# Kernel optimization log

Hardware: AMD Instinct MI355X
Metric: run time of the kernel (lower is better)

The kernel has to match this reference:

```python
import jax, jax.numpy as jnp
import numpy as np

H = 128        # num_hidden
NIN = 384      # num_in
FF = 4 * H
SCALE = 30.0
EPS = 1e-5


def _gelu(x):
    return jax.nn.gelu(x, approximate=False)


def _layernorm(x, g, b):
    mu = jnp.mean(x, axis=-1, keepdims=True)
    var = jnp.var(x, axis=-1, keepdims=True)
    return (x - mu) * jax.lax.rsqrt(var + EPS) * g + b


def setup_inputs() -> dict:
    key = jax.random.key(0)
    ks = jax.random.split(key, 12)
    B, N, K = 4, 2048, 48
    s = lambda fan_in: 1.0 / np.sqrt(fan_in)
    inp = {
        "h_V": jax.random.normal(ks[0], (B, N, H), jnp.float32),
        "h_E": jax.random.normal(ks[1], (B, N, K, NIN), jnp.float32),
        "mask_V": jnp.ones((B, N), jnp.float32),
        "mask_attend": jnp.ones((B, N, K), jnp.float32),
        "W1_w": jax.random.uniform(ks[2], (H + NIN, H), jnp.float32, -s(H + NIN), s(H + NIN)),
        "W1_b": jnp.zeros((H,), jnp.float32),
        "W2_w": jax.random.uniform(ks[3], (H, H), jnp.float32, -s(H), s(H)),
        "W2_b": jnp.zeros((H,), jnp.float32),
        "W3_w": jax.random.uniform(ks[4], (H, H), jnp.float32, -s(H), s(H)),
        "W3_b": jnp.zeros((H,), jnp.float32),
        "Win_w": jax.random.uniform(ks[5], (H, FF), jnp.float32, -s(H), s(H)),
        "Win_b": jnp.zeros((FF,), jnp.float32),
        "Wout_w": jax.random.uniform(ks[6], (FF, H), jnp.float32, -s(FF), s(FF)),
        "Wout_b": jnp.zeros((H,), jnp.float32),
        "ln1_g": jnp.ones((H,), jnp.float32),
        "ln1_b": jnp.zeros((H,), jnp.float32),
        "ln2_g": jnp.ones((H,), jnp.float32),
        "ln2_b": jnp.zeros((H,), jnp.float32),
    }
    return inp


def reference(h_V, h_E, mask_V, mask_attend,
              W1_w, W1_b, W2_w, W2_b, W3_w, W3_b,
              Win_w, Win_b, Wout_w, Wout_b,
              ln1_g, ln1_b, ln2_g, ln2_b):
    B, N, K, _ = h_E.shape
    # expand node feats over K neighbors and concat with edge feats -> [B,N,K,H+NIN]
    h_V_expand = jnp.broadcast_to(h_V[:, :, None, :], (B, N, K, h_V.shape[-1]))
    h_EV = jnp.concatenate([h_V_expand, h_E], axis=-1)
    # edge MLP: 3 linears, 2 GELUs
    h_message = _gelu(h_EV @ W1_w + W1_b)
    h_message = _gelu(h_message @ W2_w + W2_b)
    h_message = h_message @ W3_w + W3_b
    h_message = mask_attend[..., None] * h_message
    dh = jnp.sum(h_message, axis=-2) / SCALE  # [B,N,H]
    h = _layernorm(h_V + dh, ln1_g, ln1_b)
    # position-wise FFN
    dh = _gelu(h @ Win_w + Win_b) @ Wout_w + Wout_b
    h = _layernorm(h + dh, ln2_g, ln2_b)
    h = mask_V[..., None] * h
    return h
```

## Files before the change

### kernel.cpp

```cpp
#include <hip/hip_runtime.h>
#include <hip/hip_bf16.h>

#define Hh    128
#define NINc  384
#define KN    48
#define FFd   512
#define NNODE 8192

typedef __attribute__((ext_vector_type(8))) short short8v;
typedef __attribute__((ext_vector_type(4))) float f32x4;

__device__ __forceinline__ short f2bf1(float f){
  union { __hip_bfloat16 h; short s; } c; c.h = __float2bfloat16(f);
  return c.s;
}
__device__ __forceinline__ unsigned pk_bf16(float lo, float hi){
  union { __hip_bfloat162 h; unsigned u; } c;
  c.h = __float22bfloat162_rn(make_float2(lo, hi));
  return c.u;
}

__device__ __forceinline__ float gelu_f(float x){
  float t = 0.7978845608028654f * x * (1.0f + 0.044715f * x * x);
  float e = __expf(2.0f * t);
  return x * (1.0f - 1.0f / (e + 1.0f));
}

__device__ __forceinline__ void bar_lds(){
  asm volatile("s_waitcnt lgkmcnt(0)\n\ts_barrier" ::: "memory");
}

__global__ void prep_weights(const float* __restrict__ W1, const float* __restrict__ W2,
                             const float* __restrict__ W3, const float* __restrict__ Win,
                             const float* __restrict__ Wout,
                             short* __restrict__ w1vT, short* __restrict__ w1p,
                             short* __restrict__ w2p,  short* __restrict__ w3p,
                             short* __restrict__ winT, short* __restrict__ woutT)
{
  int i = blockIdx.x * 256 + threadIdx.x;
  if (i < 16384){ int n = i / 128, k = i % 128; w1vT[i] = f2bf1(W1[k*128 + n]); return; }
  i -= 16384;
  if (i < 49152){
    int n = i / 6144, r = i % 6144;
    int ks = r / 512, r2 = r % 512;
    int lane = r2 / 8, j = r2 % 8;
    int qq = lane >> 4, arow = lane & 15;
    w1p[i] = f2bf1(W1[(128 + ks*32 + qq*8 + j)*128 + n*16 + arow]); return;
  }
  i -= 49152;
  if (i < 16384){
    int n = i / 2048, r = i % 2048;
    int ks = r / 512, r2 = r % 512;
    int lane = r2 / 8, j = r2 % 8;
    int qq = lane >> 4, arow = lane & 15;
    w2p[i] = f2bf1(W2[(ks*32 + qq*8 + j)*128 + n*16 + arow]); return;
  }
  i -= 16384;
  if (i < 16384){
    int n = i / 2048, r = i % 2048;
    int ks = r / 512, r2 = r % 512;
    int lane = r2 / 8, j = r2 % 8;
    int qq = lane >> 4, arow = lane & 15;
    w3p[i] = f2bf1(W3[(ks*32 + qq*8 + j)*128 + n*16 + arow]); return;
  }
  i -= 16384;
  if (i < 65536){ int n = i / 128, k = i % 128; winT[i] = f2bf1(Win[k*512 + n]); return; }
  i -= 65536;
  if (i < 65536){ int n = i / 512, k = i % 512; woutT[i] = f2bf1(Wout[k*128 + n]); return; }
}

__global__ __launch_bounds__(256,4) void np_kernel(
    const float* __restrict__ hV, const short* __restrict__ w1vT,
    const float* __restrict__ b1, float* __restrict__ npart)
{
  const int row0 = blockIdx.x * 32;
  const int tid = threadIdx.x, lane = tid & 63, wv = tid >> 6;
  __shared__ __attribute__((aligned(16))) short Xs[32][Hh + 8];

  const float4* src = (const float4*)(hV + (size_t)row0 * Hh);
  #pragma unroll
  for (int j = 0; j < 4; ++j){
    int idx = tid + 256*j;
    int r = idx >> 5, c4 = idx & 31;
    float4 v = src[idx];
    *(uint2*)&Xs[r][c4*4] = make_uint2(pk_bf16(v.x,v.y), pk_bf16(v.z,v.w));
  }
  __syncthreads();

  const int arow = lane & 15, kgrp = (lane >> 4) * 8;
  const int col0 = wv * 32, ccol = lane & 15, crow0 = (lane >> 4) * 4;

  f32x4 acc[2][2];
  #pragma unroll
  for (int m = 0; m < 2; ++m) for (int n = 0; n < 2; ++n) acc[m][n] = (f32x4){0.f,0.f,0.f,0.f};

  const short8v* Bw = (const short8v*)w1vT;
  #pragma unroll
  for (int ks = 0; ks < 4; ++ks){
    int kb = ks*32 + kgrp;
    short8v b0 = Bw[(col0 + arow)*16      + (kb >> 3)];
    short8v b1f = Bw[(col0 + 16 + arow)*16 + (kb >> 3)];
    #pragma unroll
    for (int m = 0; m < 2; ++m){
      short8v a = *(const short8v*)&Xs[m*16 + arow][kb];
      acc[m][0] = __builtin_amdgcn_mfma_f32_16x16x32_bf16(a, b0,  acc[m][0], 0,0,0);
      acc[m][1] = __builtin_amdgcn_mfma_f32_16x16x32_bf16(a, b1f, acc[m][1], 0,0,0);
    }
  }
  #pragma unroll
  for (int m = 0; m < 2; ++m) for (int n = 0; n < 2; ++n){
    int colg = col0 + n*16 + ccol;
    float bb = b1[colg];
    #pragma unroll
    for (int r = 0; r < 4; ++r)
      npart[(size_t)(row0 + m*16 + crow0 + r)*Hh + colg] = acc[m][n][r] + bb;
  }
}

__global__ __launch_bounds__(256,4) void edge_kernel(
    const float* __restrict__ hE, const float* __restrict__ hV,
    const float* __restrict__ maskA, const float* __restrict__ npart,
    const short* __restrict__ w1p, const short* __restrict__ w2p,
    const short* __restrict__ w3p,
    const float* __restrict__ b2, const float* __restrict__ b3,
    float* __restrict__ out)
{
  const int node = blockIdx.x;
  const int tid = threadIdx.x, lane = tid & 63, wv = tid >> 6;
  const int e = lane & 15, q = lane >> 4;
  const int n0 = wv * 32;

  __shared__ __attribute__((aligned(16))) short Et[KN][NINc + 8];
  short (*M1)[136] = (short (*)[136])&Et[0][0];
  short (*M2)[136] = (short (*)[136])(&Et[0][0] + KN*136);

  {
    const float4* src = (const float4*)(hE + (size_t)node * (KN*NINc));
    float4 pfa[9], pfb[9];
    #pragma unroll
    for (int j = 0; j < 9; ++j){
      pfa[j] = src[2*tid     + 512*j];
      pfb[j] = src[2*tid + 1 + 512*j];
    }
    #pragma unroll
    for (int j = 0; j < 9; ++j){
      int idx = 2*tid + 512*j;
      int r = idx / 96, c = idx - r*96;
      uint4 u;
      u.x = pk_bf16(pfa[j].x, pfa[j].y);
      u.y = pk_bf16(pfa[j].z, pfa[j].w);
      u.z = pk_bf16(pfb[j].x, pfb[j].y);
      u.w = pk_bf16(pfb[j].z, pfb[j].w);
      *(uint4*)&Et[r][c*4] = u;
    }
  }

  const float4 npv0 = *(const float4*)(npart + (size_t)node*Hh + n0 + 4*q);
  const float4 npv1 = *(const float4*)(npart + (size_t)node*Hh + n0 + 16 + 4*q);
  const float mk0 = maskA[node*KN + e];
  const float mk1 = maskA[node*KN + 16 + e];
  const float mk2 = maskA[node*KN + 32 + e];

  bar_lds();

  const f32x4 Z = (f32x4){0.f,0.f,0.f,0.f};

  #define WR_M(DST, ACC, ET, COLB, BV)  { short4 s;                 \
    s.x = f2bf1(gelu_f(ACC[0] + BV.x));                             \
    s.y = f2bf1(gelu_f(ACC[1] + BV.y));                             \
    s.z = f2bf1(gelu_f(ACC[2] + BV.z));                             \
    s.w = f2bf1(gelu_f(ACC[3] + BV.w));                             \
    *(short4*)&DST[16*ET + e][COLB + 4*q] = s; }

  f32x4 a00=Z, a10=Z, a20=Z, a01=Z, a11=Z, a21=Z;
  {
    const short8v* B1 = (const short8v*)w1p;
    #pragma unroll
    for (int ks = 0; ks < 12; ++ks){
      short8v f0 = B1[((2*wv  )*12 + ks)*64 + lane];
      short8v f1 = B1[((2*wv+1)*12 + ks)*64 + lane];
      int kb = ks*32 + q*8;
      short8v t0 = *(const short8v*)&Et[e][kb];
      short8v t1 = *(const short8v*)&Et[16 + e][kb];
      short8v t2 = *(const short8v*)&Et[32 + e][kb];
      a00 = __builtin_amdgcn_mfma_f32_16x16x32_bf16(f0, t0, a00, 0,0,0);
      a10 = __builtin_amdgcn_mfma_f32_16x16x32_bf16(f0, t1, a10, 0,0,0);
      a20 = __builtin_amdgcn_mfma_f32_16x16x32_bf16(f0, t2, a20, 0,0,0);
      a01 = __builtin_amdgcn_mfma_f32_16x16x32_bf16(f1, t0, a01, 0,0,0);
      a11 = __builtin_amdgcn_mfma_f32_16x16x32_bf16(f1, t1, a11, 0,0,0);
      a21 = __builtin_amdgcn_mfma_f32_16x16x32_bf16(f1, t2, a21, 0,0,0);
    }
  }
  bar_lds();

  const float4 b2v0 = *(const float4*)(b2 + n0 + 4*q);
  const float4 b2v1 = *(const float4*)(b2 + n0 + 16 + 4*q);

  {
    WR_M(M1, a00, 0, n0,      npv0)  WR_M(M1, a10, 1, n0,      npv0)
    WR_M(M1, a20, 2, n0,      npv0)  WR_M(M1, a01, 0, n0 + 16, npv1)
    WR_M(M1, a11, 1, n0 + 16, npv1)  WR_M(M1, a21, 2, n0 + 16, npv1)
  }
  bar_lds();

  {
    f32x4 c00=Z, c10=Z, c20=Z, c01=Z, c11=Z, c21=Z;
    const short8v* B2f = (const short8v*)w2p;
    #pragma unroll
    for (int ks = 0; ks < 4; ++ks){
      short8v f0 = B2f[((2*wv  )*4 + ks)*64 + lane];
      short8v f1 = B2f[((2*wv+1)*4 + ks)*64 + lane];
      int kb = ks*32 + q*8;
      short8v t0 = *(const short8v*)&M1[e][kb];
      short8v t1 = *(const short8v*)&M1[16 + e][kb];
      short8v t2 = *(const short8v*)&M1[32 + e][kb];
      c00 = __builtin_amdgcn_mfma_f32_16x16x32_bf16(f0, t0, c00, 0,0,0);
      c10 = __builtin_amdgcn_mfma_f32_16x16x32_bf16(f0, t1, c10, 0,0,0);
      c20 = __builtin_amdgcn_mfma_f32_16x16x32_bf16(f0, t2, c20, 0,0,0);
      c01 = __builtin_amdgcn_mfma_f32_16x16x32_bf16(f1, t0, c01, 0,0,0);
      c11 = __builtin_amdgcn_mfma_f32_16x16x32_bf16(f1, t1, c11, 0,0,0);
      c21 = __builtin_amdgcn_mfma_f32_16x16x32_bf16(f1, t2, c21, 0,0,0);
    }
    WR_M(M2, c00, 0, n0,      b2v0)  WR_M(M2, c10, 1, n0,      b2v0)
    WR_M(M2, c20, 2, n0,      b2v0)  WR_M(M2, c01, 0, n0 + 16, b2v1)
    WR_M(M2, c11, 1, n0 + 16, b2v1)  WR_M(M2, c21, 2, n0 + 16, b2v1)
  }

  const float4 b3v0 = *(const float4*)(b3 + n0 + 4*q);
  const float4 b3v1 = *(const float4*)(b3 + n0 + 16 + 4*q);
  const float4 hvv0 = *(const float4*)(hV + (size_t)node*Hh + n0 + 4*q);
  const float4 hvv1 = *(const float4*)(hV + (size_t)node*Hh + n0 + 16 + 4*q);

  bar_lds();

  {
    f32x4 d00=Z, d10=Z, d20=Z, d01=Z, d11=Z, d21=Z;
    const short8v* B3f = (const short8v*)w3p;
    #pragma unroll
    for (int ks = 0; ks < 4; ++ks){
      short8v f0 = B3f[((2*wv  )*4 + ks)*64 + lane];
      short8v f1 = B3f[((2*wv+1)*4 + ks)*64 + lane];
      int kb = ks*32 + q*8;
      short8v t0 = *(const short8v*)&M2[e][kb];
      short8v t1 = *(const short8v*)&M2[16 + e][kb];
      short8v t2 = *(const short8v*)&M2[32 + e][kb];
      d00 = __builtin_amdgcn_mfma_f32_16x16x32_bf16(f0, t0, d00, 0,0,0);
      d10 = __builtin_amdgcn_mfma_f32_16x16x32_bf16(f0, t1, d10, 0,0,0);
      d20 = __builtin_amdgcn_mfma_f32_16x16x32_bf16(f0, t2, d20, 0,0,0);
      d01 = __builtin_amdgcn_mfma_f32_16x16x32_bf16(f1, t0, d01, 0,0,0);
      d11 = __builtin_amdgcn_mfma_f32_16x16x32_bf16(f1, t1, d11, 0,0,0);
      d21 = __builtin_amdgcn_mfma_f32_16x16x32_bf16(f1, t2, d21, 0,0,0);
    }
    f32x4 v0, v1;
    #pragma unroll
    for (int r = 0; r < 4; ++r){
      v0[r] = (d00[r] + b3v0[r])*mk0 + (d10[r] + b3v0[r])*mk1 + (d20[r] + b3v0[r])*mk2;
      v1[r] = (d01[r] + b3v1[r])*mk0 + (d11[r] + b3v1[r])*mk1 + (d21[r] + b3v1[r])*mk2;
    }
    #pragma unroll
    for (int s = 1; s <= 8; s <<= 1){
      #pragma unroll
      for (int r = 0; r < 4; ++r){
        v0[r] += __shfl_xor(v0[r], s);
        v1[r] += __shfl_xor(v1[r], s);
      }
    }
    if (e == 0){
      float4 o0, o1;
      o0.x = hvv0.x + v0[0]*(1.0f/30.0f); o0.y = hvv0.y + v0[1]*(1.0f/30.0f);
      o0.z = hvv0.z + v0[2]*(1.0f/30.0f); o0.w = hvv0.w + v0[3]*(1.0f/30.0f);
      o1.x = hvv1.x + v1[0]*(1.0f/30.0f); o1.y = hvv1.y + v1[1]*(1.0f/30.0f);
      o1.z = hvv1.z + v1[2]*(1.0f/30.0f); o1.w = hvv1.w + v1[3]*(1.0f/30.0f);
      *(float4*)(out + (size_t)node*Hh + n0 + 4*q)      = o0;
      *(float4*)(out + (size_t)node*Hh + n0 + 16 + 4*q) = o1;
    }
  }
  #undef WR_M
}

__global__ __launch_bounds__(256,2) void ffn_kernel(
    const float* __restrict__ ln1g, const float* __restrict__ ln1b,
    const short* __restrict__ winT, const float* __restrict__ bin,
    const short* __restrict__ woutT, const float* __restrict__ bout,
    const float* __restrict__ ln2g, const float* __restrict__ ln2b,
    const float* __restrict__ maskV, float* __restrict__ io)
{
  const int row0 = blockIdx.x * 32;
  const int tid = threadIdx.x, lane = tid & 63, wv = tid >> 6;
  __shared__ __attribute__((aligned(16))) short Xs[32][Hh + 8];
  __shared__ __attribute__((aligned(16))) float Rs[32][Hh + 4];
  __shared__ __attribute__((aligned(16))) short Hs[32][FFd + 8];

  const int arow = lane & 15, kgrp = (lane >> 4) * 8;
  const int ccol = lane & 15, crow0 = (lane >> 4) * 4;

  {
    int r = tid >> 3, cb = (tid & 7) * 16;
    const float4* xp = (const float4*)(io + (size_t)(row0 + r)*Hh + cb);
    float xv[16];
    #pragma unroll
    for (int j = 0; j < 4; ++j){
      float4 v = xp[j];
      xv[j*4+0]=v.x; xv[j*4+1]=v.y; xv[j*4+2]=v.z; xv[j*4+3]=v.w;
    }
    float sum = 0.f, sq = 0.f;
    #pragma unroll
    for (int j = 0; j < 16; ++j){ sum += xv[j]; sq += xv[j]*xv[j]; }
    #pragma unroll
    for (int d = 1; d < 8; d <<= 1){ sum += __shfl_xor(sum, d); sq += __shfl_xor(sq, d); }
    float mu = sum * (1.0f/128.0f);
    float var = sq * (1.0f/128.0f) - mu*mu;
    float rstd = rsqrtf(var + 1e-5f);
    #pragma unroll
    for (int j = 0; j < 16; ++j){
      int c = cb + j;
      float xn = (xv[j] - mu) * rstd * ln1g[c] + ln1b[c];
      Xs[r][c] = f2bf1(xn);
      Rs[r][c] = xn;
    }
  }
  __syncthreads();

  {
    f32x4 acc[2][8];
    #pragma unroll
    for (int m = 0; m < 2; ++m) for (int n = 0; n < 8; ++n) acc[m][n] = (f32x4){0.f,0.f,0.f,0.f};
    const short8v* Bw = (const short8v*)winT;
    #pragma unroll
    for (int ks = 0; ks < 4; ++ks){
      int kb = ks*32 + kgrp;
      short8v a0 = *(const short8v*)&Xs[arow][kb];
      short8v a1 = *(const short8v*)&Xs[16 + arow][kb];
      #pragma unroll
      for (int n = 0; n < 8; ++n){
        short8v b = Bw[(wv*128 + n*16 + arow)*16 + (kb >> 3)];
        acc[0][n] = __builtin_amdgcn_mfma_f32_16x16x32_bf16(a0,b,acc[0][n],0,0,0);
        acc[1][n] = __builtin_amdgcn_mfma_f32_16x16x32_bf16(a1,b,acc[1][n],0,0,0);
      }
    }
    #pragma unroll
    for (int m = 0; m < 2; ++m) for (int n = 0; n < 8; ++n){
      int colg = wv*128 + n*16 + ccol;
      float bb = bin[colg];
      #pragma unroll
      for (int r = 0; r < 4; ++r)
        Hs[m*16 + crow0 + r][colg] = f2bf1(gelu_f(acc[m][n][r] + bb));
    }
  }
  __syncthreads();

  {
    f32x4 acc[2][2];
    #pragma unroll
    for (int m = 0; m < 2; ++m) for (int n = 0; n < 2; ++n) acc[m][n] = (f32x4){0.f,0.f,0.f,0.f};
    const short8v* Bw = (const short8v*)woutT;
    #pragma unroll
    for (int ks = 0; ks < 16; ++ks){
      int kb = ks*32 + kgrp;
      short8v a0 = *(const short8v*)&Hs[arow][kb];
      short8v a1 = *(const short8v*)&Hs[16 + arow][kb];
      short8v b0 = Bw[(wv*32 + arow)*64      + (kb >> 3)];
      short8v b1f = Bw[(wv*32 + 16 + arow)*64 + (kb >> 3)];
      acc[0][0] = __builtin_amdgcn_mfma_f32_16x16x32_bf16(a0,b0, acc[0][0],0,0,0);
      acc[1][0] = __builtin_amdgcn_mfma_f32_16x16x32_bf16(a1,b0, acc[1][0],0,0,0);
      acc[0][1] = __builtin_amdgcn_mfma_f32_16x16x32_bf16(a0,b1f,acc[0][1],0,0,0);
      acc[1][1] = __builtin_amdgcn_mfma_f32_16x16x32_bf16(a1,b1f,acc[1][1],0,0,0);
    }
    #pragma unroll
    for (int m = 0; m < 2; ++m) for (int n = 0; n < 2; ++n){
      int colg = wv*32 + n*16 + ccol;
      float bb = bout[colg];
      #pragma unroll
      for (int r = 0; r < 4; ++r){
        int rr = m*16 + crow0 + r;
        Rs[rr][colg] = Rs[rr][colg] + acc[m][n][r] + bb;
      }
    }
  }
  __syncthreads();

  {
    int r = tid >> 3, cb = (tid & 7) * 16;
    float xv[16];
    #pragma unroll
    for (int j = 0; j < 16; ++j) xv[j] = Rs[r][cb + j];
    float sum = 0.f, sq = 0.f;
    #pragma unroll
    for (int j = 0; j < 16; ++j){ sum += xv[j]; sq += xv[j]*xv[j]; }
    #pragma unroll
    for (int d = 1; d < 8; d <<= 1){ sum += __shfl_xor(sum, d); sq += __shfl_xor(sq, d); }
    float mu = sum * (1.0f/128.0f);
    float var = sq * (1.0f/128.0f) - mu*mu;
    float rstd = rsqrtf(var + 1e-5f);
    float mv = maskV[row0 + r];
    float* op = io + (size_t)(row0 + r)*Hh + cb;
    #pragma unroll
    for (int j = 0; j < 4; ++j){
      float4 o;
      o.x = ((xv[j*4+0] - mu)*rstd*ln2g[cb+j*4+0] + ln2b[cb+j*4+0]) * mv;
      o.y = ((xv[j*4+1] - mu)*rstd*ln2g[cb+j*4+1] + ln2b[cb+j*4+1]) * mv;
      o.z = ((xv[j*4+2] - mu)*rstd*ln2g[cb+j*4+2] + ln2b[cb+j*4+2]) * mv;
      o.w = ((xv[j*4+3] - mu)*rstd*ln2g[cb+j*4+3] + ln2b[cb+j*4+3]) * mv;
      ((float4*)op)[j] = o;
    }
  }
}

extern "C" void kernel_launch(void* const* d_in, const int* in_sizes, int n_in,
                              void* d_out, int out_size, void* d_ws, size_t ws_size,
                              hipStream_t stream)
{
  const float* hV    = (const float*)d_in[0];
  const float* hE    = (const float*)d_in[1];
  const float* maskV = (const float*)d_in[2];
  const float* maskA = (const float*)d_in[3];
  const float* W1w   = (const float*)d_in[4];
  const float* W1b   = (const float*)d_in[5];
  const float* W2w   = (const float*)d_in[6];
  const float* W2b   = (const float*)d_in[7];
  const float* W3w   = (const float*)d_in[8];
  const float* W3b   = (const float*)d_in[9];
  const float* Winw  = (const float*)d_in[10];
  const float* Winb  = (const float*)d_in[11];
  const float* Woutw = (const float*)d_in[12];
  const float* Woutb = (const float*)d_in[13];
  const float* l1g   = (const float*)d_in[14];
  const float* l1b   = (const float*)d_in[15];
  const float* l2g   = (const float*)d_in[16];
  const float* l2b   = (const float*)d_in[17];

  char* ws = (char*)d_ws;
  size_t off = 0;
  float* npart = (float*)(ws + off); off += (size_t)NNODE * Hh * 4;
  short* w1vT  = (short*)(ws + off); off += 16384*2;
  short* w1p   = (short*)(ws + off); off += 49152*2;
  short* w2p   = (short*)(ws + off); off += 16384*2;
  short* w3p   = (short*)(ws + off); off += 16384*2;
  short* winT  = (short*)(ws + off); off += 65536*2;
  short* woutT = (short*)(ws + off); off += 65536*2;
  if (ws_size < off) return;

  prep_weights<<<896, 256, 0, stream>>>(W1w, W2w, W3w, Winw, Woutw,
                                        w1vT, w1p, w2p, w3p, winT, woutT);
  np_kernel<<<NNODE/32, 256, 0, stream>>>(hV, w1vT, W1b, npart);
  edge_kernel<<<NNODE, 256, 0, stream>>>(hE, hV, maskA, npart,
                                         w1p, w2p, w3p, W2b, W3b, (float*)d_out);
  ffn_kernel<<<NNODE/32, 256, 0, stream>>>(l1g, l1b, winT, Winb, woutT, Woutb,
                                           l2g, l2b, maskV, (float*)d_out);
}
```

Before: 204.7 us.

## Warp-specialize edge kernel with producer waves double-buffering hE over persistent nodes

Edge kernel now processes 32 nodes per block with 512 threads: four producer waves load and bf16-convert the next node's hE into a double-buffered LDS tile while four consumer waves run the three-layer MLP on the current node. W1 fragments are held in registers across all nodes instead of reloaded per node. This aims to overlap global memory streaming with MFMA work, at the cost of a smaller grid (256 blocks), extra barriers per node, and heavy register use from the cached W1 fragments.

```diff
diff --git a/kernel.cpp b/kernel.cpp
--- a/kernel.cpp
+++ b/kernel.cpp
@@ -6,6 +6,8 @@
 #define KN    48
 #define FFd   512
 #define NNODE 8192
+#define NPB   32
+#define EGRID (NNODE/NPB)
 
 typedef __attribute__((ext_vector_type(8))) short short8v;
 typedef __attribute__((ext_vector_type(4))) float f32x4;
@@ -117,7 +119,7 @@
   }
 }
 
-__global__ __launch_bounds__(256,4) void edge_kernel(
+__global__ __launch_bounds__(512,2) void edge_kernel(
     const float* __restrict__ hE, const float* __restrict__ hV,
     const float* __restrict__ maskA, const float* __restrict__ npart,
     const short* __restrict__ w1p, const short* __restrict__ w2p,
@@ -125,45 +127,64 @@
     const float* __restrict__ b2, const float* __restrict__ b3,
     float* __restrict__ out)
 {
-  const int node = blockIdx.x;
+  const int base = blockIdx.x * NPB;
   const int tid = threadIdx.x, lane = tid & 63, wv = tid >> 6;
+  const bool cons = (wv < 4), prod = !cons;
   const int e = lane & 15, q = lane >> 4;
-  const int n0 = wv * 32;
-
-  __shared__ __attribute__((aligned(16))) short Et[KN][NINc + 8];
-  short (*M1)[136] = (short (*)[136])&Et[0][0];
-  short (*M2)[136] = (short (*)[136])(&Et[0][0] + KN*136);
-
-  {
-    const float4* src = (const float4*)(hE + (size_t)node * (KN*NINc));
-    float4 pfa[9], pfb[9];
+  const int n0 = (wv & 3) * 32;
+  const int tid2 = tid & 255;
+
+  __shared__ __attribute__((aligned(16))) short Et[2][KN][NINc + 8];
+  __shared__ __attribute__((aligned(16))) short M1[KN][136];
+  __shared__ __attribute__((aligned(16))) short M2[KN][136];
+
+  float4 pfa[9], pfb[9];
+  auto LOADP = [&](int nn){
+    const float4* src = (const float4*)(hE + (size_t)nn * (KN*NINc));
     #pragma unroll
     for (int j = 0; j < 9; ++j){
-      pfa[j] = src[2*tid     + 512*j];
-      pfb[j] = src[2*tid + 1 + 512*j];
-    }
+      pfa[j] = src[2*tid2     + 512*j];
+      pfb[j] = src[2*tid2 + 1 + 512*j];
+    }
+  };
+  auto STOREP = [&](int buf){
     #pragma unroll
     for (int j = 0; j < 9; ++j){
-      int idx = 2*tid + 512*j;
+      int idx = 2*tid2 + 512*j;
       int r = idx / 96, c = idx - r*96;
       uint4 u;
       u.x = pk_bf16(pfa[j].x, pfa[j].y);
       u.y = pk_bf16(pfa[j].z, pfa[j].w);
       u.z = pk_bf16(pfb[j].x, pfb[j].y);
       u.w = pk_bf16(pfb[j].z, pfb[j].w);
-      *(uint4*)&Et[r][c*4] = u;
-    }
-  }
-
-  const float4 npv0 = *(const float4*)(npart + (size_t)node*Hh + n0 + 4*q);
-  const float4 npv1 = *(const float4*)(npart + (size_t)node*Hh + n0 + 16 + 4*q);
-  const float mk0 = maskA[node*KN + e];
-  const float mk1 = maskA[node*KN + 16 + e];
-  const float mk2 = maskA[node*KN + 32 + e];
-
+      *(uint4*)&Et[buf][r][c*4] = u;
+    }
+  };
+
+  short8v w1f0[12], w1f1[12];
+  float4 b2v0, b2v1, b3v0, b3v1;
+  if (cons){
+    const short8v* B1 = (const short8v*)w1p;
+    #pragma unroll
+    for (int ks = 0; ks < 12; ++ks){
+      w1f0[ks] = B1[((2*(wv&3)  )*12 + ks)*64 + lane];
+      w1f1[ks] = B1[((2*(wv&3)+1)*12 + ks)*64 + lane];
+    }
+    b2v0 = *(const float4*)(b2 + n0 + 4*q);
+    b2v1 = *(const float4*)(b2 + n0 + 16 + 4*q);
+    b3v0 = *(const float4*)(b3 + n0 + 4*q);
+    b3v1 = *(const float4*)(b3 + n0 + 16 + 4*q);
+  }
+
+  if (prod){
+    LOADP(base);
+    STOREP(0);
+    LOADP(base + 1);
+  }
   bar_lds();
 
   const f32x4 Z = (f32x4){0.f,0.f,0.f,0.f};
+  int cur = 0;
 
   #define WR_M(DST, ACC, ET, COLB, BV)  { short4 s;                 \
     s.x = f2bf1(gelu_f(ACC[0] + BV.x));                             \
@@ -172,108 +193,113 @@
     s.w = f2bf1(gelu_f(ACC[3] + BV.w));                             \
     *(short4*)&DST[16*ET + e][COLB + 4*q] = s; }
 
-  f32x4 a00=Z, a10=Z, a20=Z, a01=Z, a11=Z, a21=Z;
-  {
-    const short8v* B1 = (const short8v*)w1p;
-    #pragma unroll
-    for (int ks = 0; ks < 12; ++ks){
-      short8v f0 = B1[((2*wv  )*12 + ks)*64 + lane];
-      short8v f1 = B1[((2*wv+1)*12 + ks)*64 + lane];
-      int kb = ks*32 + q*8;
-      short8v t0 = *(const short8v*)&Et[e][kb];
-      short8v t1 = *(const short8v*)&Et[16 + e][kb];
-      short8v t2 = *(const short8v*)&Et[32 + e][kb];
-      a00 = __builtin_amdgcn_mfma_f32_16x16x32_bf16(f0, t0, a00, 0,0,0);
-      a10 = __builtin_amdgcn_mfma_f32_16x16x32_bf16(f0, t1, a10, 0,0,0);
-      a20 = __builtin_amdgcn_mfma_f32_16x16x32_bf16(f0, t2, a20, 0,0,0);
-      a01 = __builtin_amdgcn_mfma_f32_16x16x32_bf16(f1, t0, a01, 0,0,0);
-      a11 = __builtin_amdgcn_mfma_f32_16x16x32_bf16(f1, t1, a11, 0,0,0);
-      a21 = __builtin_amdgcn_mfma_f32_16x16x32_bf16(f1, t2, a21, 0,0,0);
-    }
-  }
-  bar_lds();
-
-  const float4 b2v0 = *(const float4*)(b2 + n0 + 4*q);
-  const float4 b2v1 = *(const float4*)(b2 + n0 + 16 + 4*q);
-
-  {
-    WR_M(M1, a00, 0, n0,      npv0)  WR_M(M1, a10, 1, n0,      npv0)
-    WR_M(M1, a20, 2, n0,      npv0)  WR_M(M1, a01, 0, n0 + 16, npv1)
-    WR_M(M1, a11, 1, n0 + 16, npv1)  WR_M(M1, a21, 2, n0 + 16, npv1)
-  }
-  bar_lds();
-
-  {
-    f32x4 c00=Z, c10=Z, c20=Z, c01=Z, c11=Z, c21=Z;
-    const short8v* B2f = (const short8v*)w2p;
-    #pragma unroll
-    for (int ks = 0; ks < 4; ++ks){
-      short8v f0 = B2f[((2*wv  )*4 + ks)*64 + lane];
-      short8v f1 = B2f[((2*wv+1)*4 + ks)*64 + lane];
-      int kb = ks*32 + q*8;
-      short8v t0 = *(const short8v*)&M1[e][kb];
-      short8v t1 = *(const short8v*)&M1[16 + e][kb];
-      short8v t2 = *(const short8v*)&M1[32 + e][kb];
-      c00 = __builtin_amdgcn_mfma_f32_16x16x32_bf16(f0, t0, c00, 0,0,0);
-      c10 = __builtin_amdgcn_mfma_f32_16x16x32_bf16(f0, t1, c10, 0,0,0);
-      c20 = __builtin_amdgcn_mfma_f32_16x16x32_bf16(f0, t2, c20, 0,0,0);
-      c01 = __builtin_amdgcn_mfma_f32_16x16x32_bf16(f1, t0, c01, 0,0,0);
-      c11 = __builtin_amdgcn_mfma_f32_16x16x32_bf16(f1, t1, c11, 0,0,0);
-      c21 = __builtin_amdgcn_mfma_f32_16x16x32_bf16(f1, t2, c21, 0,0,0);
-    }
-    WR_M(M2, c00, 0, n0,      b2v0)  WR_M(M2, c10, 1, n0,      b2v0)
-    WR_M(M2, c20, 2, n0,      b2v0)  WR_M(M2, c01, 0, n0 + 16, b2v1)
-    WR_M(M2, c11, 1, n0 + 16, b2v1)  WR_M(M2, c21, 2, n0 + 16, b2v1)
-  }
-
-  const float4 b3v0 = *(const float4*)(b3 + n0 + 4*q);
-  const float4 b3v1 = *(const float4*)(b3 + n0 + 16 + 4*q);
-  const float4 hvv0 = *(const float4*)(hV + (size_t)node*Hh + n0 + 4*q);
-  const float4 hvv1 = *(const float4*)(hV + (size_t)node*Hh + n0 + 16 + 4*q);
-
-  bar_lds();
-
-  {
-    f32x4 d00=Z, d10=Z, d20=Z, d01=Z, d11=Z, d21=Z;
-    const short8v* B3f = (const short8v*)w3p;
-    #pragma unroll
-    for (int ks = 0; ks < 4; ++ks){
-      short8v f0 = B3f[((2*wv  )*4 + ks)*64 + lane];
-      short8v f1 = B3f[((2*wv+1)*4 + ks)*64 + lane];
-      int kb = ks*32 + q*8;
-      short8v t0 = *(const short8v*)&M2[e][kb];
-      short8v t1 = *(const short8v*)&M2[16 + e][kb];
-      short8v t2 = *(const short8v*)&M2[32 + e][kb];
-      d00 = __builtin_amdgcn_mfma_f32_16x16x32_bf16(f0, t0, d00, 0,0,0);
-      d10 = __builtin_amdgcn_mfma_f32_16x16x32_bf16(f0, t1, d10, 0,0,0);
-      d20 = __builtin_amdgcn_mfma_f32_16x16x32_bf16(f0, t2, d20, 0,0,0);
-      d01 = __builtin_amdgcn_mfma_f32_16x16x32_bf16(f1, t0, d01, 0,0,0);
-      d11 = __builtin_amdgcn_mfma_f32_16x16x32_bf16(f1, t1, d11, 0,0,0);
-      d21 = __builtin_amdgcn_mfma_f32_16x16x32_bf16(f1, t2, d21, 0,0,0);
-    }
-    f32x4 v0, v1;
-    #pragma unroll
-    for (int r = 0; r < 4; ++r){
-      v0[r] = (d00[r] + b3v0[r])*mk0 + (d10[r] + b3v0[r])*mk1 + (d20[r] + b3v0[r])*mk2;
-      v1[r] = (d01[r] + b3v1[r])*mk0 + (d11[r] + b3v1[r])*mk1 + (d21[r] + b3v1[r])*mk2;
-    }
-    #pragma unroll
-    for (int s = 1; s <= 8; s <<= 1){
+  for (int t = 0; t < NPB; ++t){
+    const int node = base + t;
+
+    float4 npv0, npv1, hvv0, hvv1;
+    float mk0 = 0.f, mk1 = 0.f, mk2 = 0.f;
+
+    if (cons){
+      npv0 = *(const float4*)(npart + (size_t)node*Hh + n0 + 4*q);
+      npv1 = *(const float4*)(npart + (size_t)node*Hh + n0 + 16 + 4*q);
+      mk0 = maskA[node*KN + e];
+      mk1 = maskA[node*KN + 16 + e];
+      mk2 = maskA[node*KN + 32 + e];
+      hvv0 = *(const float4*)(hV + (size_t)node*Hh + n0 + 4*q);
+      hvv1 = *(const float4*)(hV + (size_t)node*Hh + n0 + 16 + 4*q);
+
+      f32x4 a00=Z, a10=Z, a20=Z, a01=Z, a11=Z, a21=Z;
+      #pragma unroll
+      for (int ks = 0; ks < 12; ++ks){
+        int kb = ks*32 + q*8;
+        short8v t0 = *(const short8v*)&Et[cur][e][kb];
+        short8v t1 = *(const short8v*)&Et[cur][16 + e][kb];
+        short8v t2 = *(const short8v*)&Et[cur][32 + e][kb];
+        a00 = __builtin_amdgcn_mfma_f32_16x16x32_bf16(w1f0[ks], t0, a00, 0,0,0);
+        a10 = __builtin_amdgcn_mfma_f32_16x16x32_bf16(w1f0[ks], t1, a10, 0,0,0);
+        a20 = __builtin_amdgcn_mfma_f32_16x16x32_bf16(w1f0[ks], t2, a20, 0,0,0);
+        a01 = __builtin_amdgcn_mfma_f32_16x16x32_bf16(w1f1[ks], t0, a01, 0,0,0);
+        a11 = __builtin_amdgcn_mfma_f32_16x16x32_bf16(w1f1[ks], t1, a11, 0,0,0);
+        a21 = __builtin_amdgcn_mfma_f32_16x16x32_bf16(w1f1[ks], t2, a21, 0,0,0);
+      }
+      WR_M(M1, a00, 0, n0,      npv0)  WR_M(M1, a10, 1, n0,      npv0)
+      WR_M(M1, a20, 2, n0,      npv0)  WR_M(M1, a01, 0, n0 + 16, npv1)
+      WR_M(M1, a11, 1, n0 + 16, npv1)  WR_M(M1, a21, 2, n0 + 16, npv1)
+    }
+    bar_lds();
+
+    if (cons){
+      f32x4 c00=Z, c10=Z, c20=Z, c01=Z, c11=Z, c21=Z;
+      const short8v* B2f = (const short8v*)w2p;
+      #pragma unroll
+      for (int ks = 0; ks < 4; ++ks){
+        short8v f0 = B2f[((2*(wv&3)  )*4 + ks)*64 + lane];
+        short8v f1 = B2f[((2*(wv&3)+1)*4 + ks)*64 + lane];
+        int kb = ks*32 + q*8;
+        short8v t0 = *(const short8v*)&M1[e][kb];
+        short8v t1 = *(const short8v*)&M1[16 + e][kb];
+        short8v t2 = *(const short8v*)&M1[32 + e][kb];
+        c00 = __builtin_amdgcn_mfma_f32_16x16x32_bf16(f0, t0, c00, 0,0,0);
+        c10 = __builtin_amdgcn_mfma_f32_16x16x32_bf16(f0, t1, c10, 0,0,0);
+        c20 = __builtin_amdgcn_mfma_f32_16x16x32_bf16(f0, t2, c20, 0,0,0);
+        c01 = __builtin_amdgcn_mfma_f32_16x16x32_bf16(f1, t0, c01, 0,0,0);
+        c11 = __builtin_amdgcn_mfma_f32_16x16x32_bf16(f1, t1, c11, 0,0,0);
+        c21 = __builtin_amdgcn_mfma_f32_16x16x32_bf16(f1, t2, c21, 0,0,0);
+      }
+      WR_M(M2, c00, 0, n0,      b2v0)  WR_M(M2, c10, 1, n0,      b2v0)
+      WR_M(M2, c20, 2, n0,      b2v0)  WR_M(M2, c01, 0, n0 + 16, b2v1)
+      WR_M(M2, c11, 1, n0 + 16, b2v1)  WR_M(M2, c21, 2, n0 + 16, b2v1)
+    }
+    bar_lds();
+
+    if (cons){
+      f32x4 d00=Z, d10=Z, d20=Z, d01=Z, d11=Z, d21=Z;
+      const short8v* B3f = (const short8v*)w3p;
+      #pragma unroll
+      for (int ks = 0; ks < 4; ++ks){
+        short8v f0 = B3f[((2*(wv&3)  )*4 + ks)*64 + lane];
+        short8v f1 = B3f[((2*(wv&3)+1)*4 + ks)*64 + lane];
+        int kb = ks*32 + q*8;
+        short8v t0 = *(const short8v*)&M2[e][kb];
+        short8v t1 = *(const short8v*)&M2[16 + e][kb];
+        short8v t2 = *(const short8v*)&M2[32 + e][kb];
+        d00 = __builtin_amdgcn_mfma_f32_16x16x32_bf16(f0, t0, d00, 0,0,0);
+        d10 = __builtin_amdgcn_mfma_f32_16x16x32_bf16(f0, t1, d10, 0,0,0);
+        d20 = __builtin_amdgcn_mfma_f32_16x16x32_bf16(f0, t2, d20, 0,0,0);
+        d01 = __builtin_amdgcn_mfma_f32_16x16x32_bf16(f1, t0, d01, 0,0,0);
+        d11 = __builtin_amdgcn_mfma_f32_16x16x32_bf16(f1, t1, d11, 0,0,0);
+        d21 = __builtin_amdgcn_mfma_f32_16x16x32_bf16(f1, t2, d21, 0,0,0);
+      }
+      f32x4 v0, v1;
       #pragma unroll
       for (int r = 0; r < 4; ++r){
-        v0[r] += __shfl_xor(v0[r], s);
-        v1[r] += __shfl_xor(v1[r], s);
-      }
-    }
-    if (e == 0){
-      float4 o0, o1;
-      o0.x = hvv0.x + v0[0]*(1.0f/30.0f); o0.y = hvv0.y + v0[1]*(1.0f/30.0f);
-      o0.z = hvv0.z + v0[2]*(1.0f/30.0f); o0.w = hvv0.w + v0[3]*(1.0f/30.0f);
-      o1.x = hvv1.x + v1[0]*(1.0f/30.0f); o1.y = hvv1.y + v1[1]*(1.0f/30.0f);
-      o1.z = hvv1.z + v1[2]*(1.0f/30.0f); o1.w = hvv1.w + v1[3]*(1.0f/30.0f);
-      *(float4*)(out + (size_t)node*Hh + n0 + 4*q)      = o0;
-      *(float4*)(out + (size_t)node*Hh + n0 + 16 + 4*q) = o1;
-    }
+        v0[r] = (d00[r] + b3v0[r])*mk0 + (d10[r] + b3v0[r])*mk1 + (d20[r] + b3v0[r])*mk2;
+        v1[r] = (d01[r] + b3v1[r])*mk0 + (d11[r] + b3v1[r])*mk1 + (d21[r] + b3v1[r])*mk2;
+      }
+      #pragma unroll
+      for (int s = 1; s <= 8; s <<= 1){
+        #pragma unroll
+        for (int r = 0; r < 4; ++r){
+          v0[r] += __shfl_xor(v0[r], s);
+          v1[r] += __shfl_xor(v1[r], s);
+        }
+      }
+      if (e == 0){
+        float4 o0, o1;
+        o0.x = hvv0.x + v0[0]*(1.0f/30.0f); o0.y = hvv0.y + v0[1]*(1.0f/30.0f);
+        o0.z = hvv0.z + v0[2]*(1.0f/30.0f); o0.w = hvv0.w + v0[3]*(1.0f/30.0f);
+        o1.x = hvv1.x + v1[0]*(1.0f/30.0f); o1.y = hvv1.y + v1[1]*(1.0f/30.0f);
+        o1.z = hvv1.z + v1[2]*(1.0f/30.0f); o1.w = hvv1.w + v1[3]*(1.0f/30.0f);
+        *(float4*)(out + (size_t)node*Hh + n0 + 4*q)      = o0;
+        *(float4*)(out + (size_t)node*Hh + n0 + 16 + 4*q) = o1;
+      }
+    }
+    if (prod && t + 1 < NPB){
+      STOREP(cur ^ 1);
+      if (t + 2 < NPB) LOADP(base + t + 2);
+    }
+    bar_lds();
+    cur ^= 1;
   }
   #undef WR_M
 }
@@ -443,7 +469,7 @@
   prep_weights<<<896, 256, 0, stream>>>(W1w, W2w, W3w, Winw, Woutw,
                                         w1vT, w1p, w2p, w3p, winT, woutT);
   np_kernel<<<NNODE/32, 256, 0, stream>>>(hV, w1vT, W1b, npart);
-  edge_kernel<<<NNODE, 256, 0, stream>>>(hE, hV, maskA, npart,
+  edge_kernel<<<EGRID, 512, 0, stream>>>(hE, hV, maskA, npart,
                                          w1p, w2p, w3p, W2b, W3b, (float*)d_out);
   ffn_kernel<<<NNODE/32, 256, 0, stream>>>(l1g, l1b, winT, Winb, woutT, Woutb,
                                            l2g, l2b, maskV, (float*)d_out);
```

Measured after the change: 378.8 us. 1.85x slower.

## Load edge features directly into LDS as fp32 with XOR swizzle

Applied to the files above, without the earlier changes.

Replaces the register-staged global load plus bf16 conversion with direct global-to-LDS loads of the fp32 edge tile, using an XOR swizzle on 16-byte segments to avoid bank conflicts. Conversion to bf16 now happens when each MFMA operand is read from LDS. This doubles the LDS footprint per block (72KB vs ~37KB), so the launch bound drops to 2 blocks per CU, lowering occupancy and thus the latency hiding available for the HBM-bound edge stream.

```diff
diff --git a/kernel.cpp b/kernel.cpp
--- a/kernel.cpp
+++ b/kernel.cpp
@@ -18,6 +18,12 @@
   union { __hip_bfloat162 h; unsigned u; } c;
   c.h = __float22bfloat162_rn(make_float2(lo, hi));
   return c.u;
+}
+__device__ __forceinline__ short8v pack8(float4 a, float4 b){
+  union { short8v s; unsigned u[4]; } r;
+  r.u[0] = pk_bf16(a.x, a.y); r.u[1] = pk_bf16(a.z, a.w);
+  r.u[2] = pk_bf16(b.x, b.y); r.u[3] = pk_bf16(b.z, b.w);
+  return r.s;
 }
 
 __device__ __forceinline__ float gelu_f(float x){
@@ -117,7 +123,7 @@
   }
 }
 
-__global__ __launch_bounds__(256,4) void edge_kernel(
+__global__ __launch_bounds__(256,2) void edge_kernel(
     const float* __restrict__ hE, const float* __restrict__ hV,
     const float* __restrict__ maskA, const float* __restrict__ npart,
     const short* __restrict__ w1p, const short* __restrict__ w2p,
@@ -130,28 +136,24 @@
   const int e = lane & 15, q = lane >> 4;
   const int n0 = wv * 32;
 
-  __shared__ __attribute__((aligned(16))) short Et[KN][NINc + 8];
-  short (*M1)[136] = (short (*)[136])&Et[0][0];
-  short (*M2)[136] = (short (*)[136])(&Et[0][0] + KN*136);
-
-  {
-    const float4* src = (const float4*)(hE + (size_t)node * (KN*NINc));
-    float4 pfa[9], pfb[9];
-    #pragma unroll
-    for (int j = 0; j < 9; ++j){
-      pfa[j] = src[2*tid     + 512*j];
-      pfb[j] = src[2*tid + 1 + 512*j];
-    }
-    #pragma unroll
-    for (int j = 0; j < 9; ++j){
-      int idx = 2*tid + 512*j;
-      int r = idx / 96, c = idx - r*96;
-      uint4 u;
-      u.x = pk_bf16(pfa[j].x, pfa[j].y);
-      u.y = pk_bf16(pfa[j].z, pfa[j].w);
-      u.z = pk_bf16(pfb[j].x, pfb[j].y);
-      u.w = pk_bf16(pfb[j].z, pfb[j].w);
-      *(uint4*)&Et[r][c*4] = u;
+  __shared__ __attribute__((aligned(16))) float Etf[KN * NINc];
+  short (*M1)[136] = (short (*)[136])&Etf[0];
+  short (*M2)[136] = (short (*)[136])((short*)&Etf[0] + KN*136);
+
+  {
+    const char* gb = (const char*)(hE + (size_t)node * (KN*NINc));
+    #pragma unroll
+    for (int j = 0; j < 18; ++j){
+      int chunk = wv*18 + j;
+      int S = chunk*64 + lane;
+      int r = S / 96, sp = S - r*96;
+      int gs = sp ^ (r & 7);
+      __builtin_amdgcn_global_load_lds(
+        (const __attribute__((address_space(1))) unsigned int*)
+            (gb + ((size_t)r*96 + gs)*16),
+        (__attribute__((address_space(3))) unsigned int*)
+            ((char*)&Etf[0] + chunk*1024),
+        16, 0, 0);
     }
   }
 
@@ -161,7 +163,7 @@
   const float mk1 = maskA[node*KN + 16 + e];
   const float mk2 = maskA[node*KN + 32 + e];
 
-  bar_lds();
+  __syncthreads();
 
   const f32x4 Z = (f32x4){0.f,0.f,0.f,0.f};
 
@@ -172,6 +174,10 @@
     s.w = f2bf1(gelu_f(ACC[3] + BV.w));                             \
     *(short4*)&DST[16*ET + e][COLB + 4*q] = s; }
 
+  #define RD_F(ROW, S0)  pack8(                                     \
+      *(const float4*)&Etf[(ROW)*384 + (((S0)  ) ^ ((ROW)&7))*4],   \
+      *(const float4*)&Etf[(ROW)*384 + (((S0)+1) ^ ((ROW)&7))*4])
+
   f32x4 a00=Z, a10=Z, a20=Z, a01=Z, a11=Z, a21=Z;
   {
     const short8v* B1 = (const short8v*)w1p;
@@ -179,10 +185,10 @@
     for (int ks = 0; ks < 12; ++ks){
       short8v f0 = B1[((2*wv  )*12 + ks)*64 + lane];
       short8v f1 = B1[((2*wv+1)*12 + ks)*64 + lane];
-      int kb = ks*32 + q*8;
-      short8v t0 = *(const short8v*)&Et[e][kb];
-      short8v t1 = *(const short8v*)&Et[16 + e][kb];
-      short8v t2 = *(const short8v*)&Et[32 + e][kb];
+      int s0 = ks*8 + q*2;
+      short8v t0 = RD_F(e,      s0);
+      short8v t1 = RD_F(16 + e, s0);
+      short8v t2 = RD_F(32 + e, s0);
       a00 = __builtin_amdgcn_mfma_f32_16x16x32_bf16(f0, t0, a00, 0,0,0);
       a10 = __builtin_amdgcn_mfma_f32_16x16x32_bf16(f0, t1, a10, 0,0,0);
       a20 = __builtin_amdgcn_mfma_f32_16x16x32_bf16(f0, t2, a20, 0,0,0);
@@ -276,6 +282,7 @@
     }
   }
   #undef WR_M
+  #undef RD_F
 }
 
 __global__ __launch_bounds__(256,2) void ffn_kernel(
```

Measured after the change: 236.3 us. +15.4%, slower.

## Sum over neighbors before W3 linear and pipeline edge feature loads

Applied to the files above, without the earlier changes.

Uses linearity of the third edge linear: the masked sum over the K neighbors is taken after the second GELU, and W3 is applied once per node in a new dh_kernel along with the bias scaled by the mask sum. This removes the per-edge W3 matmul and the M2 LDS round trip from the edge kernel. The hE staging is also split into three column chunks so global loads of the next chunk overlap the first-layer MFMAs on the current one. The cost is an extra kernel launch, an fp32 scratch buffer written and read per node, and bf16 rounding of the neighbor-summed activations.

```diff
diff --git a/kernel.cpp b/kernel.cpp
--- a/kernel.cpp
+++ b/kernel.cpp
@@ -34,7 +34,7 @@
                              const float* __restrict__ W3, const float* __restrict__ Win,
                              const float* __restrict__ Wout,
                              short* __restrict__ w1vT, short* __restrict__ w1p,
-                             short* __restrict__ w2p,  short* __restrict__ w3p,
+                             short* __restrict__ w2p,  short* __restrict__ w3T,
                              short* __restrict__ winT, short* __restrict__ woutT)
 {
   int i = blockIdx.x * 256 + threadIdx.x;
@@ -56,13 +56,7 @@
     w2p[i] = f2bf1(W2[(ks*32 + qq*8 + j)*128 + n*16 + arow]); return;
   }
   i -= 16384;
-  if (i < 16384){
-    int n = i / 2048, r = i % 2048;
-    int ks = r / 512, r2 = r % 512;
-    int lane = r2 / 8, j = r2 % 8;
-    int qq = lane >> 4, arow = lane & 15;
-    w3p[i] = f2bf1(W3[(ks*32 + qq*8 + j)*128 + n*16 + arow]); return;
-  }
+  if (i < 16384){ int n = i / 128, k = i % 128; w3T[i] = f2bf1(W3[k*128 + n]); return; }
   i -= 16384;
   if (i < 65536){ int n = i / 128, k = i % 128; winT[i] = f2bf1(Win[k*512 + n]); return; }
   i -= 65536;
@@ -118,12 +112,11 @@
 }
 
 __global__ __launch_bounds__(256,4) void edge_kernel(
-    const float* __restrict__ hE, const float* __restrict__ hV,
+    const float* __restrict__ hE,
     const float* __restrict__ maskA, const float* __restrict__ npart,
     const short* __restrict__ w1p, const short* __restrict__ w2p,
-    const short* __restrict__ w3p,
-    const float* __restrict__ b2, const float* __restrict__ b3,
-    float* __restrict__ out)
+    const float* __restrict__ b2,
+    float* __restrict__ sbuf, float* __restrict__ smaskbuf)
 {
   const int node = blockIdx.x;
   const int tid = threadIdx.x, lane = tid & 63, wv = tid >> 6;
@@ -132,51 +125,44 @@
 
   __shared__ __attribute__((aligned(16))) short Et[KN][NINc + 8];
   short (*M1)[136] = (short (*)[136])&Et[0][0];
-  short (*M2)[136] = (short (*)[136])(&Et[0][0] + KN*136);
-
-  {
-    const float4* src = (const float4*)(hE + (size_t)node * (KN*NINc));
-    float4 pfa[9], pfb[9];
-    #pragma unroll
-    for (int j = 0; j < 9; ++j){
-      pfa[j] = src[2*tid     + 512*j];
-      pfb[j] = src[2*tid + 1 + 512*j];
-    }
-    #pragma unroll
-    for (int j = 0; j < 9; ++j){
-      int idx = 2*tid + 512*j;
-      int r = idx / 96, c = idx - r*96;
-      uint4 u;
-      u.x = pk_bf16(pfa[j].x, pfa[j].y);
-      u.y = pk_bf16(pfa[j].z, pfa[j].w);
-      u.z = pk_bf16(pfb[j].x, pfb[j].y);
-      u.w = pk_bf16(pfb[j].z, pfb[j].w);
-      *(uint4*)&Et[r][c*4] = u;
-    }
-  }
+
+  const float4* src = (const float4*)(hE + (size_t)node * (KN*NINc));
+  float4 pf[6];
+
+  auto LOADC = [&](int c){
+    #pragma unroll
+    for (int j = 0; j < 6; ++j){
+      int idx = tid + 256*j;
+      int r = idx >> 5, c4 = idx & 31;
+      pf[j] = src[r*96 + c*32 + c4];
+    }
+  };
+  auto STOREC = [&](int c){
+    #pragma unroll
+    for (int j = 0; j < 6; ++j){
+      int idx = tid + 256*j;
+      int r = idx >> 5, c4 = idx & 31;
+      *(uint2*)&Et[r][c*128 + c4*4] =
+        make_uint2(pk_bf16(pf[j].x, pf[j].y), pk_bf16(pf[j].z, pf[j].w));
+    }
+  };
 
   const float4 npv0 = *(const float4*)(npart + (size_t)node*Hh + n0 + 4*q);
   const float4 npv1 = *(const float4*)(npart + (size_t)node*Hh + n0 + 16 + 4*q);
+  const float4 b2v0 = *(const float4*)(b2 + n0 + 4*q);
+  const float4 b2v1 = *(const float4*)(b2 + n0 + 16 + 4*q);
   const float mk0 = maskA[node*KN + e];
   const float mk1 = maskA[node*KN + 16 + e];
   const float mk2 = maskA[node*KN + 32 + e];
 
-  bar_lds();
-
   const f32x4 Z = (f32x4){0.f,0.f,0.f,0.f};
-
-  #define WR_M(DST, ACC, ET, COLB, BV)  { short4 s;                 \
-    s.x = f2bf1(gelu_f(ACC[0] + BV.x));                             \
-    s.y = f2bf1(gelu_f(ACC[1] + BV.y));                             \
-    s.z = f2bf1(gelu_f(ACC[2] + BV.z));                             \
-    s.w = f2bf1(gelu_f(ACC[3] + BV.w));                             \
-    *(short4*)&DST[16*ET + e][COLB + 4*q] = s; }
-
   f32x4 a00=Z, a10=Z, a20=Z, a01=Z, a11=Z, a21=Z;
-  {
-    const short8v* B1 = (const short8v*)w1p;
-    #pragma unroll
-    for (int ks = 0; ks < 12; ++ks){
+  const short8v* B1 = (const short8v*)w1p;
+
+  auto G1C = [&](int c){
+    #pragma unroll
+    for (int kk = 0; kk < 4; ++kk){
+      int ks = c*4 + kk;
       short8v f0 = B1[((2*wv  )*12 + ks)*64 + lane];
       short8v f1 = B1[((2*wv+1)*12 + ks)*64 + lane];
       int kb = ks*32 + q*8;
@@ -190,17 +176,33 @@
       a11 = __builtin_amdgcn_mfma_f32_16x16x32_bf16(f1, t1, a11, 0,0,0);
       a21 = __builtin_amdgcn_mfma_f32_16x16x32_bf16(f1, t2, a21, 0,0,0);
     }
-  }
+  };
+
+  LOADC(0);
+  STOREC(0);
+  LOADC(1);
   bar_lds();
-
-  const float4 b2v0 = *(const float4*)(b2 + n0 + 4*q);
-  const float4 b2v1 = *(const float4*)(b2 + n0 + 16 + 4*q);
-
-  {
-    WR_M(M1, a00, 0, n0,      npv0)  WR_M(M1, a10, 1, n0,      npv0)
-    WR_M(M1, a20, 2, n0,      npv0)  WR_M(M1, a01, 0, n0 + 16, npv1)
-    WR_M(M1, a11, 1, n0 + 16, npv1)  WR_M(M1, a21, 2, n0 + 16, npv1)
-  }
+  G1C(0);
+  STOREC(1);
+  LOADC(2);
+  bar_lds();
+  G1C(1);
+  STOREC(2);
+  bar_lds();
+  G1C(2);
+  bar_lds();
+
+  #define WR_M(ACC, ET, COLB, BV)  { short4 s;                      \
+    s.x = f2bf1(gelu_f(ACC[0] + BV.x));                             \
+    s.y = f2bf1(gelu_f(ACC[1] + BV.y));                             \
+    s.z = f2bf1(gelu_f(ACC[2] + BV.z));                             \
+    s.w = f2bf1(gelu_f(ACC[3] + BV.w));                             \
+    *(short4*)&M1[16*ET + e][COLB + 4*q] = s; }
+
+  WR_M(a00, 0, n0,      npv0)  WR_M(a10, 1, n0,      npv0)
+  WR_M(a20, 2, n0,      npv0)  WR_M(a01, 0, n0 + 16, npv1)
+  WR_M(a11, 1, n0 + 16, npv1)  WR_M(a21, 2, n0 + 16, npv1)
+  #undef WR_M
   bar_lds();
 
   {
@@ -221,61 +223,86 @@
       c11 = __builtin_amdgcn_mfma_f32_16x16x32_bf16(f1, t1, c11, 0,0,0);
       c21 = __builtin_amdgcn_mfma_f32_16x16x32_bf16(f1, t2, c21, 0,0,0);
     }
-    WR_M(M2, c00, 0, n0,      b2v0)  WR_M(M2, c10, 1, n0,      b2v0)
-    WR_M(M2, c20, 2, n0,      b2v0)  WR_M(M2, c01, 0, n0 + 16, b2v1)
-    WR_M(M2, c11, 1, n0 + 16, b2v1)  WR_M(M2, c21, 2, n0 + 16, b2v1)
-  }
-
-  const float4 b3v0 = *(const float4*)(b3 + n0 + 4*q);
-  const float4 b3v1 = *(const float4*)(b3 + n0 + 16 + 4*q);
-  const float4 hvv0 = *(const float4*)(hV + (size_t)node*Hh + n0 + 4*q);
-  const float4 hvv1 = *(const float4*)(hV + (size_t)node*Hh + n0 + 16 + 4*q);
-
-  bar_lds();
-
-  {
-    f32x4 d00=Z, d10=Z, d20=Z, d01=Z, d11=Z, d21=Z;
-    const short8v* B3f = (const short8v*)w3p;
-    #pragma unroll
-    for (int ks = 0; ks < 4; ++ks){
-      short8v f0 = B3f[((2*wv  )*4 + ks)*64 + lane];
-      short8v f1 = B3f[((2*wv+1)*4 + ks)*64 + lane];
-      int kb = ks*32 + q*8;
-      short8v t0 = *(const short8v*)&M2[e][kb];
-      short8v t1 = *(const short8v*)&M2[16 + e][kb];
-      short8v t2 = *(const short8v*)&M2[32 + e][kb];
-      d00 = __builtin_amdgcn_mfma_f32_16x16x32_bf16(f0, t0, d00, 0,0,0);
-      d10 = __builtin_amdgcn_mfma_f32_16x16x32_bf16(f0, t1, d10, 0,0,0);
-      d20 = __builtin_amdgcn_mfma_f32_16x16x32_bf16(f0, t2, d20, 0,0,0);
-      d01 = __builtin_amdgcn_mfma_f32_16x16x32_bf16(f1, t0, d01, 0,0,0);
-      d11 = __builtin_amdgcn_mfma_f32_16x16x32_bf16(f1, t1, d11, 0,0,0);
-      d21 = __builtin_amdgcn_mfma_f32_16x16x32_bf16(f1, t2, d21, 0,0,0);
-    }
-    f32x4 v0, v1;
+    float sv0[4], sv1[4];
     #pragma unroll
     for (int r = 0; r < 4; ++r){
-      v0[r] = (d00[r] + b3v0[r])*mk0 + (d10[r] + b3v0[r])*mk1 + (d20[r] + b3v0[r])*mk2;
-      v1[r] = (d01[r] + b3v1[r])*mk0 + (d11[r] + b3v1[r])*mk1 + (d21[r] + b3v1[r])*mk2;
-    }
+      sv0[r] = gelu_f(c00[r] + b2v0[r])*mk0 + gelu_f(c10[r] + b2v0[r])*mk1
+             + gelu_f(c20[r] + b2v0[r])*mk2;
+      sv1[r] = gelu_f(c01[r] + b2v1[r])*mk0 + gelu_f(c11[r] + b2v1[r])*mk1
+             + gelu_f(c21[r] + b2v1[r])*mk2;
+    }
+    float m3 = mk0 + mk1 + mk2;
     #pragma unroll
     for (int s = 1; s <= 8; s <<= 1){
       #pragma unroll
       for (int r = 0; r < 4; ++r){
-        v0[r] += __shfl_xor(v0[r], s);
-        v1[r] += __shfl_xor(v1[r], s);
+        sv0[r] += __shfl_xor(sv0[r], s);
+        sv1[r] += __shfl_xor(sv1[r], s);
       }
+      m3 += __shfl_xor(m3, s);
     }
     if (e == 0){
-      float4 o0, o1;
-      o0.x = hvv0.x + v0[0]*(1.0f/30.0f); o0.y = hvv0.y + v0[1]*(1.0f/30.0f);
-      o0.z = hvv0.z + v0[2]*(1.0f/30.0f); o0.w = hvv0.w + v0[3]*(1.0f/30.0f);
-      o1.x = hvv1.x + v1[0]*(1.0f/30.0f); o1.y = hvv1.y + v1[1]*(1.0f/30.0f);
-      o1.z = hvv1.z + v1[2]*(1.0f/30.0f); o1.w = hvv1.w + v1[3]*(1.0f/30.0f);
-      *(float4*)(out + (size_t)node*Hh + n0 + 4*q)      = o0;
-      *(float4*)(out + (size_t)node*Hh + n0 + 16 + 4*q) = o1;
-    }
-  }
-  #undef WR_M
+      float4 o0 = make_float4(sv0[0], sv0[1], sv0[2], sv0[3]);
+      float4 o1 = make_float4(sv1[0], sv1[1], sv1[2], sv1[3]);
+      *(float4*)(sbuf + (size_t)node*Hh + n0 + 4*q)      = o0;
+      *(float4*)(sbuf + (size_t)node*Hh + n0 + 16 + 4*q) = o1;
+    }
+    if (tid == 0) smaskbuf[node] = m3;
+  }
+}
+
+__global__ __launch_bounds__(256,4) void dh_kernel(
+    const float* __restrict__ hV, const float* __restrict__ sbuf,
+    const float* __restrict__ smaskbuf, const short* __restrict__ w3T,
+    const float* __restrict__ b3, float* __restrict__ out)
+{
+  const int row0 = blockIdx.x * 32;
+  const int tid = threadIdx.x, lane = tid & 63, wv = tid >> 6;
+  __shared__ __attribute__((aligned(16))) short Ss[32][Hh + 8];
+  __shared__ float smS[32];
+
+  const float4* src = (const float4*)(sbuf + (size_t)row0 * Hh);
+  #pragma unroll
+  for (int j = 0; j < 4; ++j){
+    int idx = tid + 256*j;
+    int r = idx >> 5, c4 = idx & 31;
+    float4 v = src[idx];
+    *(uint2*)&Ss[r][c4*4] = make_uint2(pk_bf16(v.x,v.y), pk_bf16(v.z,v.w));
+  }
+  if (tid < 32) smS[tid] = smaskbuf[row0 + tid];
+  __syncthreads();
+
+  const int arow = lane & 15, kgrp = (lane >> 4) * 8;
+  const int col0 = wv * 32, ccol = lane & 15, crow0 = (lane >> 4) * 4;
+
+  f32x4 acc[2][2];
+  #pragma unroll
+  for (int m = 0; m < 2; ++m) for (int n = 0; n < 2; ++n) acc[m][n] = (f32x4){0.f,0.f,0.f,0.f};
+
+  const short8v* Bw = (const short8v*)w3T;
+  #pragma unroll
+  for (int ks = 0; ks < 4; ++ks){
+    int kb = ks*32 + kgrp;
+    short8v b0 = Bw[(col0 + arow)*16      + (kb >> 3)];
+    short8v b1f = Bw[(col0 + 16 + arow)*16 + (kb >> 3)];
+    #pragma unroll
+    for (int m = 0; m < 2; ++m){
+      short8v a = *(const short8v*)&Ss[m*16 + arow][kb];
+      acc[m][0] = __builtin_amdgcn_mfma_f32_16x16x32_bf16(a, b0,  acc[m][0], 0,0,0);
+      acc[m][1] = __builtin_amdgcn_mfma_f32_16x16x32_bf16(a, b1f, acc[m][1], 0,0,0);
+    }
+  }
+  #pragma unroll
+  for (int m = 0; m < 2; ++m) for (int n = 0; n < 2; ++n){
+    int colg = col0 + n*16 + ccol;
+    float bb = b3[colg];
+    #pragma unroll
+    for (int r = 0; r < 4; ++r){
+      int rl = m*16 + crow0 + r;
+      size_t gi = (size_t)(row0 + rl)*Hh + colg;
+      out[gi] = hV[gi] + (acc[m][n][r] + bb*smS[rl]) * (1.0f/30.0f);
+    }
+  }
 }
 
 __global__ __launch_bounds__(256,2) void ffn_kernel(
@@ -432,19 +459,22 @@
   char* ws = (char*)d_ws;
   size_t off = 0;
   float* npart = (float*)(ws + off); off += (size_t)NNODE * Hh * 4;
+  float* sbuf  = (float*)(ws + off); off += (size_t)NNODE * Hh * 4;
+  float* smbuf = (float*)(ws + off); off += (size_t)NNODE * 4;
   short* w1vT  = (short*)(ws + off); off += 16384*2;
   short* w1p   = (short*)(ws + off); off += 49152*2;
   short* w2p   = (short*)(ws + off); off += 16384*2;
-  short* w3p   = (short*)(ws + off); off += 16384*2;
+  short* w3T   = (short*)(ws + off); off += 16384*2;
   short* winT  = (short*)(ws + off); off += 65536*2;
   short* woutT = (short*)(ws + off); off += 65536*2;
   if (ws_size < off) return;
 
   prep_weights<<<896, 256, 0, stream>>>(W1w, W2w, W3w, Winw, Woutw,
-                                        w1vT, w1p, w2p, w3p, winT, woutT);
+                                        w1vT, w1p, w2p, w3T, winT, woutT);
   np_kernel<<<NNODE/32, 256, 0, stream>>>(hV, w1vT, W1b, npart);
-  edge_kernel<<<NNODE, 256, 0, stream>>>(hE, hV, maskA, npart,
-                                         w1p, w2p, w3p, W2b, W3b, (float*)d_out);
+  edge_kernel<<<NNODE, 256, 0, stream>>>(hE, maskA, npart,
+                                         w1p, w2p, W2b, sbuf, smbuf);
+  dh_kernel<<<NNODE/32, 256, 0, stream>>>(hV, sbuf, smbuf, w3T, W3b, (float*)d_out);
   ffn_kernel<<<NNODE/32, 256, 0, stream>>>(l1g, l1b, winT, Winb, woutT, Woutb,
                                            l2g, l2b, maskV, (float*)d_out);
 }
```

After: 192.0 us. 6.2% less time.
